# Performance work log

Hardware: AMD Instinct MI355X
Metric: run time of the kernel (lower is better)

Reference implementation:

```python
import jax, jax.numpy as jnp
import numpy as np

N = 50000        # nodes
E = 1250000      # edges
B = 512          # graphs
DIN, DH, DOUT = 64, 64, 16


def setup_inputs() -> dict:
    key = jax.random.key(0)
    ks = jax.random.split(key, 8)
    s = lambda d: np.float32(1.0 / np.sqrt(d))
    return {
        "x": jax.random.normal(ks[0], (N, DIN), jnp.float32),
        "edge_index": jax.random.randint(ks[1], (2, E), 0, N, dtype=jnp.int32),
        "batch": jnp.sort(jax.random.randint(ks[2], (N,), 0, B, dtype=jnp.int32)),
        "W1": jax.random.normal(ks[3], (DH, DIN), jnp.float32) * s(DIN),
        "b1": jnp.zeros((DH,), jnp.float32),
        "W2": jax.random.normal(ks[4], (DH, DH), jnp.float32) * s(DH),
        "b2": jnp.zeros((DH,), jnp.float32),
        "W3": jax.random.normal(ks[5], (DH, DH), jnp.float32) * s(DH),
        "b3": jnp.zeros((DH,), jnp.float32),
        "Wl": jax.random.normal(ks[6], (DOUT, DH), jnp.float32) * s(DH),
        "bl": jnp.zeros((DOUT,), jnp.float32),
    }


def _gcn_conv(x, src, dst, norm, W, b, n):
    # PyG GCNConv: h = x W^T; out[i] = sum_{(j->i)} norm_ji * h[j] + b
    h = x @ W.T                                   # [N, DH]
    msg = h[src] * norm[:, None]                  # [E+N, DH] gather
    return jax.ops.segment_sum(msg, dst, num_segments=n) + b


def reference(x, edge_index, batch, W1, b1, W2, b2, W3, b3, Wl, bl):
    n = x.shape[0]
    loop = jnp.arange(n, dtype=edge_index.dtype)
    # add self-loops (PyG GCNConv default add_self_loops=True)
    src = jnp.concatenate([edge_index[0], loop])
    dst = jnp.concatenate([edge_index[1], loop])
    # symmetric normalization: deg^{-1/2}[src] * deg^{-1/2}[dst]
    deg = jax.ops.segment_sum(jnp.ones_like(src, jnp.float32), dst, num_segments=n)
    dinv = jax.lax.rsqrt(deg)                     # deg >= 1 thanks to self-loops
    norm = dinv[src] * dinv[dst]

    h = x
    for W, b in ((W1, b1), (W2, b2), (W3, b3)):
        h = jax.nn.relu(_gcn_conv(h, src, dst, norm, W, b, n))

    # global mean pool over each graph
    sums = jax.ops.segment_sum(h, batch, num_segments=B)          # [B, DH]
    cnts = jax.ops.segment_sum(jnp.ones((n,), jnp.float32), batch, num_segments=B)
    pooled = sums / jnp.maximum(cnts, 1.0)[:, None]
    # dropout p=0.5 is identity in eval mode
    return pooled @ Wl.T + bl                                     # [B, DOUT]
```

## Files before the change

### kernel.cpp

```cpp
#include <hip/hip_runtime.h>
#include <hip/hip_fp16.h>


#define CAPB 3072
#define BINTILE 4096

__global__ __launch_bounds__(256) void init_kernel(int* __restrict__ fctr,
                                                   const int* __restrict__ batch,
                                                   const float* __restrict__ bl,
                                                   float* __restrict__ invc,
                                                   float* __restrict__ out,
                                                   int n, int nb) {
    int t = blockIdx.x * blockDim.x + threadIdx.x;
    if (t < 512) fctr[t] = 0;
    if (t < nb) {
        int l = 0, r = n;
        while (l < r) { int m = (l + r) >> 1; if (batch[m] < t) l = m + 1; else r = m; }
        int lo = l;
        r = n;
        while (l < r) { int m = (l + r) >> 1; if (batch[m] < t + 1) l = m + 1; else r = m; }
        invc[t] = 1.0f / fmaxf((float)(l - lo), 1.0f);
#pragma unroll
        for (int o = 0; o < 16; ++o) out[t * 16 + o] = bl[o];
    }
}

__global__ __launch_bounds__(256) void bin512_kernel(const int* __restrict__ src,
                                                     const int* __restrict__ dst,
                                                     int* __restrict__ fctr,
                                                     int2* __restrict__ recs2,
                                                     int e, int n) {
    __shared__ int lcnt[512], gbase[512];
    int tid = threadIdx.x;
    int s0  = blockIdx.x * BINTILE;
    lcnt[tid] = 0;
    lcnt[tid + 256] = 0;
    __syncthreads();
    int dv[16], bk[16];
#pragma unroll
    for (int k = 0; k < 16; ++k) {
        int i = s0 + tid + k * 256;
        if (i < e) {
            dv[k] = dst[i];
            bk[k] = (int)((512LL * dv[k]) / n);
            atomicAdd(&lcnt[bk[k]], 1);
        } else {
            bk[k] = -1;
        }
    }
    __syncthreads();
#pragma unroll
    for (int j = 0; j < 2; ++j) {
        int b = tid + j * 256;
        gbase[b] = b * CAPB + atomicAdd(&fctr[b], lcnt[b]);
        lcnt[b]  = 0;
    }
    __syncthreads();
#pragma unroll
    for (int k = 0; k < 16; ++k) {
        if (bk[k] >= 0) {
            int i = s0 + tid + k * 256;
            int p = gbase[bk[k]] + atomicAdd(&lcnt[bk[k]], 1);
            if (p < (bk[k] + 1) * CAPB) recs2[p] = make_int2(src[i], dv[k]);
        }
    }
}

__global__ __launch_bounds__(256) void sortfill_mm_kernel(
    const int2* __restrict__ recs2, const int* __restrict__ fctr,
    int* __restrict__ rp, float* __restrict__ dinv, int* __restrict__ csr,
    const float* __restrict__ x, const float* __restrict__ W1,
    __half* __restrict__ t1, int n) {
    __shared__ int hist[128];
    __shared__ int lofs[129];
    __shared__ int stage[CAPB];
    __shared__ int redbuf[256];
    __shared__ float xrow[98 * 64];
    int g   = blockIdx.x;
    int N0  = (int)(((long long)n * g + 511) / 512);
    int N1  = (int)(((long long)n * (g + 1) + 511) / 512);
    int nn  = N1 - N0;
    int tid = threadIdx.x;
    int lane = tid & 63;
    int wave = tid >> 6;

    int partial = 0;
    for (int j = tid; j < g; j += 256) partial += min(fctr[j], CAPB);
    redbuf[tid] = partial;
    if (tid < 128) hist[tid] = 0;
    __syncthreads();
    for (int s = 128; s > 0; s >>= 1) {
        if (tid < s) redbuf[tid] += redbuf[tid + s];
        __syncthreads();
    }
    int base = redbuf[0];
    const int2* my = recs2 + (size_t)g * CAPB;
    int total = min(fctr[g], CAPB);
    for (int i = tid; i < total; i += 256)
        atomicAdd(&hist[my[i].y - N0], 1);
    __syncthreads();
    if (tid == 0) {
        int acc = 0;
        for (int k = 0; k < nn; ++k) { lofs[k] = acc; acc += hist[k]; }
        lofs[nn] = acc;
    }
    __syncthreads();
    if (tid < 128) hist[tid] = 0;
    __syncthreads();
    for (int i = tid; i < total; i += 256) {
        int2 rec = my[i];
        int  li  = rec.y - N0;
        int  pos = lofs[li] + atomicAdd(&hist[li], 1);
        stage[pos] = rec.x;
    }
    __syncthreads();
    for (int j = tid; j < total; j += 256) csr[base + j] = stage[j];
    if (tid < nn) {
        rp[N0 + tid]   = base + lofs[tid];
        int deg        = lofs[tid + 1] - lofs[tid];
        dinv[N0 + tid] = rsqrtf((float)(deg + 1));
    }
    if (g == 511 && tid == 0) rp[n] = base + total;

    for (int idx = tid; idx < nn * 16; idx += 256)
        ((float4*)xrow)[idx] = ((const float4*)(x + (size_t)N0 * 64))[idx];
    float4 wreg[16];
    const float4* W4 = (const float4*)(W1 + lane * 64);
#pragma unroll
    for (int q = 0; q < 16; ++q) wreg[q] = W4[q];
    __syncthreads();
    for (int li = wave; li < nn; li += 4) {
        float dv = rsqrtf((float)(lofs[li + 1] - lofs[li] + 1));
        const float4* row = (const float4*)(xrow + li * 64);
        float acc = 0.0f;
#pragma unroll
        for (int q = 0; q < 16; ++q) {
            float4 hv = row[q];
            acc += hv.x * wreg[q].x + hv.y * wreg[q].y +
                   hv.z * wreg[q].z + hv.w * wreg[q].w;
        }
        t1[(size_t)(N0 + li) * 64 + lane] = __float2half(acc * dv);
    }
}

__global__ __launch_bounds__(256) void mm_kernel(const float* __restrict__ h,
                                                 const float* __restrict__ W,
                                                 const float* __restrict__ dinv,
                                                 __half* __restrict__ t, int n) {
    __shared__ float hs[64 * 64];
    int tid  = threadIdx.x;
    int lane = tid & 63;
    int wave = tid >> 6;
    int base = blockIdx.x * 64;

    float4 wreg[16];
    const float4* W4 = (const float4*)(W + lane * 64);
#pragma unroll
    for (int q = 0; q < 16; ++q) wreg[q] = W4[q];

    int nrows = min(64, n - base);
    const float4* h4  = (const float4*)(h + (size_t)base * 64);
    float4*       hs4 = (float4*)hs;
    for (int idx = tid; idx < nrows * 16; idx += 256) hs4[idx] = h4[idx];
    __syncthreads();

    for (int r = wave * 16; r < wave * 16 + 16; ++r) {
        int i = base + r;
        if (i >= n) break;
        const float4* row = (const float4*)(hs + r * 64);
        float acc = 0.0f;
#pragma unroll
        for (int q = 0; q < 16; ++q) {
            float4 hv = row[q];
            acc += hv.x * wreg[q].x + hv.y * wreg[q].y +
                   hv.z * wreg[q].z + hv.w * wreg[q].w;
        }
        t[(size_t)i * 64 + lane] = __float2half(acc * dinv[i]);
    }
}

__global__ __launch_bounds__(256, 6) void agg_kernel(const __half* __restrict__ t,
                                                     const int* __restrict__ rp,
                                                     const int* __restrict__ cs,
                                                     const float* __restrict__ dinv,
                                                     const float* __restrict__ bias,
                                                     float* __restrict__ hout, int n) {
    int gw   = (blockIdx.x * blockDim.x + threadIdx.x) >> 6;
    int lane = threadIdx.x & 63;
    if (gw >= n) return;
    int i   = gw;
    int grp = lane >> 4;
    int fo  = (lane & 15) << 2;
    int beg = rp[i];
    int end = rp[i + 1];
    uint2 su = *(const uint2*)(t + (size_t)i * 64 + fo);
    float dv = dinv[i];
    float4 bv = *(const float4*)(bias + fo);

    int deg = end - beg;
    int len = (deg + 3) >> 2;
    int gb  = beg + grp * len;
    int ge  = min(gb + len, end);

    float4 aa[4];
    aa[0] = make_float4(0.f, 0.f, 0.f, 0.f);
    aa[1] = aa[0]; aa[2] = aa[0]; aa[3] = aa[0];
    for (int eb = gb; eb < ge; eb += 8) {
#pragma unroll
        for (int j = 0; j < 8; ++j) {
            int   ej = eb + j;
            int   ec = min(ej, end - 1);
            int   sj = cs[ec];
            uint2 u  = *(const uint2*)(t + (size_t)sj * 64 + fo);
            float m  = (ej < ge) ? 1.0f : 0.0f;
            float2 f0 = __half22float2(*(const __half2*)&u.x);
            float2 f1 = __half22float2(*(const __half2*)&u.y);
            aa[j & 3].x = fmaf(m, f0.x, aa[j & 3].x);
            aa[j & 3].y = fmaf(m, f0.y, aa[j & 3].y);
            aa[j & 3].z = fmaf(m, f1.x, aa[j & 3].z);
            aa[j & 3].w = fmaf(m, f1.y, aa[j & 3].w);
        }
    }
    float4 acc;
    acc.x = (aa[0].x + aa[1].x) + (aa[2].x + aa[3].x);
    acc.y = (aa[0].y + aa[1].y) + (aa[2].y + aa[3].y);
    acc.z = (aa[0].z + aa[1].z) + (aa[2].z + aa[3].z);
    acc.w = (aa[0].w + aa[1].w) + (aa[2].w + aa[3].w);
    acc.x += __shfl_xor(acc.x, 16, 64);
    acc.y += __shfl_xor(acc.y, 16, 64);
    acc.z += __shfl_xor(acc.z, 16, 64);
    acc.w += __shfl_xor(acc.w, 16, 64);
    acc.x += __shfl_xor(acc.x, 32, 64);
    acc.y += __shfl_xor(acc.y, 32, 64);
    acc.z += __shfl_xor(acc.z, 32, 64);
    acc.w += __shfl_xor(acc.w, 32, 64);
    if (grp == 0) {
        float2 s01 = __half22float2(*(const __half2*)&su.x);
        float2 s23 = __half22float2(*(const __half2*)&su.y);
        float4 o;
        o.x = fmaxf(fmaf(dv, acc.x + s01.x, bv.x), 0.0f);
        o.y = fmaxf(fmaf(dv, acc.y + s01.y, bv.y), 0.0f);
        o.z = fmaxf(fmaf(dv, acc.z + s23.x, bv.z), 0.0f);
        o.w = fmaxf(fmaf(dv, acc.w + s23.y, bv.w), 0.0f);
        *(float4*)(hout + (size_t)i * 64 + fo) = o;
    }
}

__global__ __launch_bounds__(256, 6) void aggfinal_kernel(const __half* __restrict__ t,
                                                          const int* __restrict__ rp,
                                                          const int* __restrict__ cs,
                                                          const float* __restrict__ dinv,
                                                          const float* __restrict__ bias,
                                                          const float* __restrict__ Wl,
                                                          const int* __restrict__ batch,
                                                          const float* __restrict__ invc,
                                                          float* __restrict__ out, int n) {
    int gw   = (blockIdx.x * blockDim.x + threadIdx.x) >> 6;
    int lane = threadIdx.x & 63;
    if (gw >= n) return;
    int i   = gw;
    int grp = lane >> 4;
    int fo  = (lane & 15) << 2;
    int beg = rp[i];
    int end = rp[i + 1];
    uint2 su = *(const uint2*)(t + (size_t)i * 64 + fo);
    float dv = dinv[i];
    float4 bv = *(const float4*)(bias + fo);

    int deg = end - beg;
    int len = (deg + 3) >> 2;
    int gb  = beg + grp * len;
    int ge  = min(gb + len, end);

    float4 aa[4];
    aa[0] = make_float4(0.f, 0.f, 0.f, 0.f);
    aa[1] = aa[0]; aa[2] = aa[0]; aa[3] = aa[0];
    for (int eb = gb; eb < ge; eb += 8) {
#pragma unroll
        for (int j = 0; j < 8; ++j) {
            int   ej = eb + j;
            int   ec = min(ej, end - 1);
            int   sj = cs[ec];
            uint2 u  = *(const uint2*)(t + (size_t)sj * 64 + fo);
            float m  = (ej < ge) ? 1.0f : 0.0f;
            float2 f0 = __half22float2(*(const __half2*)&u.x);
            float2 f1 = __half22float2(*(const __half2*)&u.y);
            aa[j & 3].x = fmaf(m, f0.x, aa[j & 3].x);
            aa[j & 3].y = fmaf(m, f0.y, aa[j & 3].y);
            aa[j & 3].z = fmaf(m, f1.x, aa[j & 3].z);
            aa[j & 3].w = fmaf(m, f1.y, aa[j & 3].w);
        }
    }
    float4 acc;
    acc.x = (aa[0].x + aa[1].x) + (aa[2].x + aa[3].x);
    acc.y = (aa[0].y + aa[1].y) + (aa[2].y + aa[3].y);
    acc.z = (aa[0].z + aa[1].z) + (aa[2].z + aa[3].z);
    acc.w = (aa[0].w + aa[1].w) + (aa[2].w + aa[3].w);
    acc.x += __shfl_xor(acc.x, 16, 64);
    acc.y += __shfl_xor(acc.y, 16, 64);
    acc.z += __shfl_xor(acc.z, 16, 64);
    acc.w += __shfl_xor(acc.w, 16, 64);
    acc.x += __shfl_xor(acc.x, 32, 64);
    acc.y += __shfl_xor(acc.y, 32, 64);
    acc.z += __shfl_xor(acc.z, 32, 64);
    acc.w += __shfl_xor(acc.w, 32, 64);

    float2 s01 = __half22float2(*(const __half2*)&su.x);
    float2 s23 = __half22float2(*(const __half2*)&su.y);
    float4 h4;
    h4.x = fmaxf(fmaf(dv, acc.x + s01.x, bv.x), 0.0f);
    h4.y = fmaxf(fmaf(dv, acc.y + s01.y, bv.y), 0.0f);
    h4.z = fmaxf(fmaf(dv, acc.z + s23.x, bv.z), 0.0f);
    h4.w = fmaxf(fmaf(dv, acc.w + s23.y, bv.w), 0.0f);

    float4 wl0 = *(const float4*)(Wl + (0 * 4 + grp) * 64 + fo);
    float4 wl1 = *(const float4*)(Wl + (1 * 4 + grp) * 64 + fo);
    float4 wl2 = *(const float4*)(Wl + (2 * 4 + grp) * 64 + fo);
    float4 wl3 = *(const float4*)(Wl + (3 * 4 + grp) * 64 + fo);
    float z0 = h4.x * wl0.x + h4.y * wl0.y + h4.z * wl0.z + h4.w * wl0.w;
    float z1 = h4.x * wl1.x + h4.y * wl1.y + h4.z * wl1.z + h4.w * wl1.w;
    float z2 = h4.x * wl2.x + h4.y * wl2.y + h4.z * wl2.z + h4.w * wl2.w;
    float z3 = h4.x * wl3.x + h4.y * wl3.y + h4.z * wl3.z + h4.w * wl3.w;
#pragma unroll
    for (int s = 1; s <= 8; s <<= 1) {
        z0 += __shfl_xor(z0, s, 64);
        z1 += __shfl_xor(z1, s, 64);
        z2 += __shfl_xor(z2, s, 64);
        z3 += __shfl_xor(z3, s, 64);
    }
    int m = lane & 15;
    if (m < 4) {
        int   b  = batch[i];
        float ic = invc[b];
        float zv = (m == 0) ? z0 : (m == 1) ? z1 : (m == 2) ? z2 : z3;
        atomicAdd(out + b * 16 + (m * 4 + grp), zv * ic);
    }
}

extern "C" void kernel_launch(void* const* d_in, const int* in_sizes, int n_in,
                              void* d_out, int out_size, void* d_ws, size_t ws_size,
                              hipStream_t stream) {
    const float* x    = (const float*)d_in[0];
    const int*   ei   = (const int*)d_in[1];
    const int*   batch= (const int*)d_in[2];
    const float* W1   = (const float*)d_in[3];
    const float* b1   = (const float*)d_in[4];
    const float* W2   = (const float*)d_in[5];
    const float* b2   = (const float*)d_in[6];
    const float* W3   = (const float*)d_in[7];
    const float* b3   = (const float*)d_in[8];
    const float* Wl   = (const float*)d_in[9];
    const float* bl   = (const float*)d_in[10];
    float* out = (float*)d_out;

    int n  = in_sizes[0] / 64;
    int e  = in_sizes[1] / 2;
    int nb = out_size / 16;

    const int* esrc = ei;
    const int* edst = ei + e;

    char* p = (char*)d_ws;
    auto carve = [&](size_t bytes) {
        char* r = p;
        p += (bytes + 255) & ~(size_t)255;
        return r;
    };
    size_t featBytes = (size_t)n * 64 * 4;
    size_t recsBytes = (size_t)512 * CAPB * 8;
    size_t bufBBytes = recsBytes > featBytes ? recsBytes : featBytes;

    float*  dinv = (float*)carve((size_t)n * 4);
    int*    rp   = (int*)  carve((size_t)(n + 1) * 4);
    int*    csr  = (int*)  carve((size_t)e * 4);
    __half* bufT = (__half*)carve((size_t)n * 64 * 2);
    float*  bufB = (float*)carve(bufBBytes);
    int*    fctr = (int*)  carve(512 * 4);
    float*  invc = (float*)carve((size_t)nb * 4);
    int2*   recs2 = (int2*)bufB;

    dim3 blk(256);
    int gBIN = (e + BINTILE - 1) / BINTILE;
    int gMM  = (n + 63) / 64;
    int gAGG = (n + 3) / 4;

    init_kernel<<<2, blk, 0, stream>>>(fctr, batch, bl, invc, out, n, nb);
    bin512_kernel<<<gBIN, blk, 0, stream>>>(esrc, edst, fctr, recs2, e, n);
    sortfill_mm_kernel<<<512, blk, 0, stream>>>(recs2, fctr, rp, dinv, csr,
                                                x, W1, bufT, n);
    agg_kernel<<<gAGG, blk, 0, stream>>>(bufT, rp, csr, dinv, b1, bufB, n);
    mm_kernel<<<gMM, blk, 0, stream>>>(bufB, W2, dinv, bufT, n);
    agg_kernel<<<gAGG, blk, 0, stream>>>(bufT, rp, csr, dinv, b2, bufB, n);
    mm_kernel<<<gMM, blk, 0, stream>>>(bufB, W3, dinv, bufT, n);
    aggfinal_kernel<<<gAGG, blk, 0, stream>>>(bufT, rp, csr, dinv, b3, Wl,
                                              batch, invc, out, n);
}
```

Before: 288.2 us.

## Fuse GCN aggregation with next-layer matmul via shared-memory tile

Replaces the separate agg and mm kernels for layers 1-2 with a single kernel that aggregates 32 nodes per 512-thread block, writes the ReLU output to shared memory, and immediately multiplies by the next weight matrix to produce the fp16 transformed features. This removes the fp32 intermediate round-trip through global memory and two kernel launches per layer. Each node is now handled by a 16-lane group instead of a full wave split four ways, so per-node edge parallelism drops, which can hurt load balance on high-degree nodes. It also adds a ping-pong fp16 buffer and gives the edge records their own workspace region.

After: 287.2 us. No clear change (-0.4%).

```diff
diff --git a/kernel.cpp b/kernel.cpp
--- a/kernel.cpp
+++ b/kernel.cpp
@@ -143,106 +143,91 @@
     }
 }
 
-__global__ __launch_bounds__(256) void mm_kernel(const float* __restrict__ h,
-                                                 const float* __restrict__ W,
-                                                 const float* __restrict__ dinv,
-                                                 __half* __restrict__ t, int n) {
-    __shared__ float hs[64 * 64];
+__global__ __launch_bounds__(512, 4) void aggmm_kernel(const __half* __restrict__ t,
+                                                       const int* __restrict__ rp,
+                                                       const int* __restrict__ cs,
+                                                       const float* __restrict__ dinv,
+                                                       const float* __restrict__ bias,
+                                                       const float* __restrict__ W,
+                                                       __half* __restrict__ tout, int n) {
+    __shared__ float hs[32 * 64];
+    __shared__ float dvs[32];
     int tid  = threadIdx.x;
     int lane = tid & 63;
     int wave = tid >> 6;
-    int base = blockIdx.x * 64;
+    int g    = lane >> 4;
+    int fo   = (lane & 15) << 2;
+    int base = blockIdx.x * 32;
+    int nl   = wave * 4 + g;
+    int i    = base + nl;
+
+    float4 a0 = make_float4(0.f, 0.f, 0.f, 0.f);
+    float4 a1 = a0;
+    float2 s01 = make_float2(0.f, 0.f), s23 = s01;
+    float  dv = 1.0f;
+
+    if (i < n) {
+        int beg = rp[i];
+        int end = rp[i + 1];
+        uint2 su = *(const uint2*)(t + (size_t)i * 64 + fo);
+        dv = dinv[i];
+        for (int eb = beg; eb < end; eb += 8) {
+#pragma unroll
+            for (int j = 0; j < 8; ++j) {
+                int   ej = eb + j;
+                int   ec = min(ej, end - 1);
+                int   sj = cs[ec];
+                uint2 u  = *(const uint2*)(t + (size_t)sj * 64 + fo);
+                float m  = (ej < end) ? 1.0f : 0.0f;
+                float2 f0 = __half22float2(*(const __half2*)&u.x);
+                float2 f1 = __half22float2(*(const __half2*)&u.y);
+                if (j & 1) {
+                    a1.x = fmaf(m, f0.x, a1.x);
+                    a1.y = fmaf(m, f0.y, a1.y);
+                    a1.z = fmaf(m, f1.x, a1.z);
+                    a1.w = fmaf(m, f1.y, a1.w);
+                } else {
+                    a0.x = fmaf(m, f0.x, a0.x);
+                    a0.y = fmaf(m, f0.y, a0.y);
+                    a0.z = fmaf(m, f1.x, a0.z);
+                    a0.w = fmaf(m, f1.y, a0.w);
+                }
+            }
+        }
+        s01 = __half22float2(*(const __half2*)&su.x);
+        s23 = __half22float2(*(const __half2*)&su.y);
+    }
+    if (i < n) {
+        float4 bv = *(const float4*)(bias + fo);
+        float4 h4;
+        h4.x = fmaxf(fmaf(dv, (a0.x + a1.x) + s01.x, bv.x), 0.0f);
+        h4.y = fmaxf(fmaf(dv, (a0.y + a1.y) + s01.y, bv.y), 0.0f);
+        h4.z = fmaxf(fmaf(dv, (a0.z + a1.z) + s23.x, bv.z), 0.0f);
+        h4.w = fmaxf(fmaf(dv, (a0.w + a1.w) + s23.y, bv.w), 0.0f);
+        *(float4*)(hs + nl * 64 + fo) = h4;
+        if ((lane & 15) == 0) dvs[nl] = dv;
+    }
+    __syncthreads();
 
     float4 wreg[16];
     const float4* W4 = (const float4*)(W + lane * 64);
 #pragma unroll
     for (int q = 0; q < 16; ++q) wreg[q] = W4[q];
-
-    int nrows = min(64, n - base);
-    const float4* h4  = (const float4*)(h + (size_t)base * 64);
-    float4*       hs4 = (float4*)hs;
-    for (int idx = tid; idx < nrows * 16; idx += 256) hs4[idx] = h4[idx];
-    __syncthreads();
-
-    for (int r = wave * 16; r < wave * 16 + 16; ++r) {
-        int i = base + r;
-        if (i >= n) break;
-        const float4* row = (const float4*)(hs + r * 64);
-        float acc = 0.0f;
-#pragma unroll
-        for (int q = 0; q < 16; ++q) {
-            float4 hv = row[q];
-            acc += hv.x * wreg[q].x + hv.y * wreg[q].y +
-                   hv.z * wreg[q].z + hv.w * wreg[q].w;
-        }
-        t[(size_t)i * 64 + lane] = __float2half(acc * dinv[i]);
-    }
-}
-
-__global__ __launch_bounds__(256, 6) void agg_kernel(const __half* __restrict__ t,
-                                                     const int* __restrict__ rp,
-                                                     const int* __restrict__ cs,
-                                                     const float* __restrict__ dinv,
-                                                     const float* __restrict__ bias,
-                                                     float* __restrict__ hout, int n) {
-    int gw   = (blockIdx.x * blockDim.x + threadIdx.x) >> 6;
-    int lane = threadIdx.x & 63;
-    if (gw >= n) return;
-    int i   = gw;
-    int grp = lane >> 4;
-    int fo  = (lane & 15) << 2;
-    int beg = rp[i];
-    int end = rp[i + 1];
-    uint2 su = *(const uint2*)(t + (size_t)i * 64 + fo);
-    float dv = dinv[i];
-    float4 bv = *(const float4*)(bias + fo);
-
-    int deg = end - beg;
-    int len = (deg + 3) >> 2;
-    int gb  = beg + grp * len;
-    int ge  = min(gb + len, end);
-
-    float4 aa[4];
-    aa[0] = make_float4(0.f, 0.f, 0.f, 0.f);
-    aa[1] = aa[0]; aa[2] = aa[0]; aa[3] = aa[0];
-    for (int eb = gb; eb < ge; eb += 8) {
-#pragma unroll
-        for (int j = 0; j < 8; ++j) {
-            int   ej = eb + j;
-            int   ec = min(ej, end - 1);
-            int   sj = cs[ec];
-            uint2 u  = *(const uint2*)(t + (size_t)sj * 64 + fo);
-            float m  = (ej < ge) ? 1.0f : 0.0f;
-            float2 f0 = __half22float2(*(const __half2*)&u.x);
-            float2 f1 = __half22float2(*(const __half2*)&u.y);
-            aa[j & 3].x = fmaf(m, f0.x, aa[j & 3].x);
-            aa[j & 3].y = fmaf(m, f0.y, aa[j & 3].y);
-            aa[j & 3].z = fmaf(m, f1.x, aa[j & 3].z);
-            aa[j & 3].w = fmaf(m, f1.y, aa[j & 3].w);
-        }
-    }
-    float4 acc;
-    acc.x = (aa[0].x + aa[1].x) + (aa[2].x + aa[3].x);
-    acc.y = (aa[0].y + aa[1].y) + (aa[2].y + aa[3].y);
-    acc.z = (aa[0].z + aa[1].z) + (aa[2].z + aa[3].z);
-    acc.w = (aa[0].w + aa[1].w) + (aa[2].w + aa[3].w);
-    acc.x += __shfl_xor(acc.x, 16, 64);
-    acc.y += __shfl_xor(acc.y, 16, 64);
-    acc.z += __shfl_xor(acc.z, 16, 64);
-    acc.w += __shfl_xor(acc.w, 16, 64);
-    acc.x += __shfl_xor(acc.x, 32, 64);
-    acc.y += __shfl_xor(acc.y, 32, 64);
-    acc.z += __shfl_xor(acc.z, 32, 64);
-    acc.w += __shfl_xor(acc.w, 32, 64);
-    if (grp == 0) {
-        float2 s01 = __half22float2(*(const __half2*)&su.x);
-        float2 s23 = __half22float2(*(const __half2*)&su.y);
-        float4 o;
-        o.x = fmaxf(fmaf(dv, acc.x + s01.x, bv.x), 0.0f);
-        o.y = fmaxf(fmaf(dv, acc.y + s01.y, bv.y), 0.0f);
-        o.z = fmaxf(fmaf(dv, acc.z + s23.x, bv.z), 0.0f);
-        o.w = fmaxf(fmaf(dv, acc.w + s23.y, bv.w), 0.0f);
-        *(float4*)(hout + (size_t)i * 64 + fo) = o;
+#pragma unroll
+    for (int rr = 0; rr < 4; ++rr) {
+        int r  = wave * 4 + rr;
+        int io = base + r;
+        if (io < n) {
+            const float4* row = (const float4*)(hs + r * 64);
+            float acc = 0.0f;
+#pragma unroll
+            for (int q = 0; q < 16; ++q) {
+                float4 hv = row[q];
+                acc += hv.x * wreg[q].x + hv.y * wreg[q].y +
+                       hv.z * wreg[q].z + hv.w * wreg[q].w;
+            }
+            tout[(size_t)io * 64 + lane] = __float2half(acc * dvs[r]);
+        }
     }
 }
 
@@ -366,32 +351,26 @@
         p += (bytes + 255) & ~(size_t)255;
         return r;
     };
-    size_t featBytes = (size_t)n * 64 * 4;
-    size_t recsBytes = (size_t)512 * CAPB * 8;
-    size_t bufBBytes = recsBytes > featBytes ? recsBytes : featBytes;
-
-    float*  dinv = (float*)carve((size_t)n * 4);
-    int*    rp   = (int*)  carve((size_t)(n + 1) * 4);
-    int*    csr  = (int*)  carve((size_t)e * 4);
-    __half* bufT = (__half*)carve((size_t)n * 64 * 2);
-    float*  bufB = (float*)carve(bufBBytes);
-    int*    fctr = (int*)  carve(512 * 4);
-    float*  invc = (float*)carve((size_t)nb * 4);
-    int2*   recs2 = (int2*)bufB;
+    float*  dinv  = (float*)carve((size_t)n * 4);
+    int*    rp    = (int*)  carve((size_t)(n + 1) * 4);
+    int*    csr   = (int*)  carve((size_t)e * 4);
+    __half* tA    = (__half*)carve((size_t)n * 64 * 2);
+    __half* tB    = (__half*)carve((size_t)n * 64 * 2);
+    int2*   recs2 = (int2*) carve((size_t)512 * CAPB * 8);
+    int*    fctr  = (int*)  carve(512 * 4);
+    float*  invc  = (float*)carve((size_t)nb * 4);
 
     dim3 blk(256);
     int gBIN = (e + BINTILE - 1) / BINTILE;
-    int gMM  = (n + 63) / 64;
+    int gFUS = (n + 31) / 32;
     int gAGG = (n + 3) / 4;
 
     init_kernel<<<2, blk, 0, stream>>>(fctr, batch, bl, invc, out, n, nb);
     bin512_kernel<<<gBIN, blk, 0, stream>>>(esrc, edst, fctr, recs2, e, n);
     sortfill_mm_kernel<<<512, blk, 0, stream>>>(recs2, fctr, rp, dinv, csr,
-                                                x, W1, bufT, n);
-    agg_kernel<<<gAGG, blk, 0, stream>>>(bufT, rp, csr, dinv, b1, bufB, n);
-    mm_kernel<<<gMM, blk, 0, stream>>>(bufB, W2, dinv, bufT, n);
-    agg_kernel<<<gAGG, blk, 0, stream>>>(bufT, rp, csr, dinv, b2, bufB, n);
-    mm_kernel<<<gMM, blk, 0, stream>>>(bufB, W3, dinv, bufT, n);
-    aggfinal_kernel<<<gAGG, blk, 0, stream>>>(bufT, rp, csr, dinv, b3, Wl,
+                                                x, W1, tA, n);
+    aggmm_kernel<<<gFUS, dim3(512), 0, stream>>>(tA, rp, csr, dinv, b1, W2, tB, n);
+    aggmm_kernel<<<gFUS, dim3(512), 0, stream>>>(tB, rp, csr, dinv, b2, W3, tA, n);
+    aggfinal_kernel<<<gAGG, blk, 0, stream>>>(tA, rp, csr, dinv, b3, Wl,
                                               batch, invc, out, n);
 }
```

## Fuse aggregation with next-layer matmul and split gathers by source half

Applied to the files above, without the earlier changes.

Replaces the separate agg and mm kernels with one aggmm kernel. Each 512-thread block aggregates 8 nodes, stages the ReLU output in shared memory, and applies the next weight matrix right away. This removes the fp32 intermediate write and read and two launches, and ping-pongs between two half-precision buffers. The gather loop makes two passes, each restricted to one half of the source nodes for cache locality, at the cost of redundant index loads and masked gathers. The final aggregation kernel also batches its index and feature loads ahead of the accumulation behind a scheduling barrier to raise memory-level parallelism.

New measurement: 440.7 us. 52.9% more time.

```diff
diff --git a/kernel.cpp b/kernel.cpp
--- a/kernel.cpp
+++ b/kernel.cpp
@@ -143,61 +143,31 @@
     }
 }
 
-__global__ __launch_bounds__(256) void mm_kernel(const float* __restrict__ h,
-                                                 const float* __restrict__ W,
-                                                 const float* __restrict__ dinv,
-                                                 __half* __restrict__ t, int n) {
-    __shared__ float hs[64 * 64];
+__global__ __launch_bounds__(512, 4) void aggmm_kernel(const __half* __restrict__ t,
+                                                       const int* __restrict__ rp,
+                                                       const int* __restrict__ cs,
+                                                       const float* __restrict__ dinv,
+                                                       const float* __restrict__ bias,
+                                                       const float* __restrict__ W,
+                                                       __half* __restrict__ tout, int n) {
+    __shared__ float hs[8 * 64];
     int tid  = threadIdx.x;
     int lane = tid & 63;
     int wave = tid >> 6;
-    int base = blockIdx.x * 64;
-
-    float4 wreg[16];
-    const float4* W4 = (const float4*)(W + lane * 64);
-#pragma unroll
-    for (int q = 0; q < 16; ++q) wreg[q] = W4[q];
-
-    int nrows = min(64, n - base);
-    const float4* h4  = (const float4*)(h + (size_t)base * 64);
-    float4*       hs4 = (float4*)hs;
-    for (int idx = tid; idx < nrows * 16; idx += 256) hs4[idx] = h4[idx];
-    __syncthreads();
-
-    for (int r = wave * 16; r < wave * 16 + 16; ++r) {
-        int i = base + r;
-        if (i >= n) break;
-        const float4* row = (const float4*)(hs + r * 64);
-        float acc = 0.0f;
-#pragma unroll
-        for (int q = 0; q < 16; ++q) {
-            float4 hv = row[q];
-            acc += hv.x * wreg[q].x + hv.y * wreg[q].y +
-                   hv.z * wreg[q].z + hv.w * wreg[q].w;
-        }
-        t[(size_t)i * 64 + lane] = __float2half(acc * dinv[i]);
-    }
-}
-
-__global__ __launch_bounds__(256, 6) void agg_kernel(const __half* __restrict__ t,
-                                                     const int* __restrict__ rp,
-                                                     const int* __restrict__ cs,
-                                                     const float* __restrict__ dinv,
-                                                     const float* __restrict__ bias,
-                                                     float* __restrict__ hout, int n) {
-    int gw   = (blockIdx.x * blockDim.x + threadIdx.x) >> 6;
-    int lane = threadIdx.x & 63;
-    if (gw >= n) return;
-    int i   = gw;
-    int grp = lane >> 4;
-    int fo  = (lane & 15) << 2;
-    int beg = rp[i];
-    int end = rp[i + 1];
-    uint2 su = *(const uint2*)(t + (size_t)i * 64 + fo);
-    float dv = dinv[i];
+    int grp  = lane >> 4;
+    int fo   = (lane & 15) << 2;
+    int base = blockIdx.x * 8;
+    int i    = base + wave;
+    int ii   = min(i, n - 1);
+
+    int beg = rp[ii];
+    int end = rp[ii + 1];
+    int deg = end - beg;
+
+    uint2 su = *(const uint2*)(t + (size_t)ii * 64 + fo);
+    float dv = dinv[ii];
     float4 bv = *(const float4*)(bias + fo);
 
-    int deg = end - beg;
     int len = (deg + 3) >> 2;
     int gb  = beg + grp * len;
     int ge  = min(gb + len, end);
@@ -205,20 +175,29 @@
     float4 aa[4];
     aa[0] = make_float4(0.f, 0.f, 0.f, 0.f);
     aa[1] = aa[0]; aa[2] = aa[0]; aa[3] = aa[0];
-    for (int eb = gb; eb < ge; eb += 8) {
-#pragma unroll
-        for (int j = 0; j < 8; ++j) {
-            int   ej = eb + j;
-            int   ec = min(ej, end - 1);
-            int   sj = cs[ec];
-            uint2 u  = *(const uint2*)(t + (size_t)sj * 64 + fo);
-            float m  = (ej < ge) ? 1.0f : 0.0f;
-            float2 f0 = __half22float2(*(const __half2*)&u.x);
-            float2 f1 = __half22float2(*(const __half2*)&u.y);
-            aa[j & 3].x = fmaf(m, f0.x, aa[j & 3].x);
-            aa[j & 3].y = fmaf(m, f0.y, aa[j & 3].y);
-            aa[j & 3].z = fmaf(m, f1.x, aa[j & 3].z);
-            aa[j & 3].w = fmaf(m, f1.y, aa[j & 3].w);
+
+    int hn = (n + 1) >> 1;
+#pragma unroll
+    for (int hf = 0; hf < 2; ++hf) {
+        int lo = hf * hn;
+        int hi = min(lo + hn, n);
+        for (int eb = gb; eb < ge; eb += 8) {
+#pragma unroll
+            for (int j = 0; j < 8; ++j) {
+                int  ej = eb + j;
+                int  ec = min(ej, end - 1);
+                int  sj = cs[ec];
+                bool ok = (ej < ge) && (sj >= lo) && (sj < hi);
+                int  sc = ok ? sj : lo;
+                uint2 u  = *(const uint2*)(t + (size_t)sc * 64 + fo);
+                float m  = ok ? 1.0f : 0.0f;
+                float2 f0 = __half22float2(*(const __half2*)&u.x);
+                float2 f1 = __half22float2(*(const __half2*)&u.y);
+                aa[j & 3].x = fmaf(m, f0.x, aa[j & 3].x);
+                aa[j & 3].y = fmaf(m, f0.y, aa[j & 3].y);
+                aa[j & 3].z = fmaf(m, f1.x, aa[j & 3].z);
+                aa[j & 3].w = fmaf(m, f1.y, aa[j & 3].w);
+            }
         }
     }
     float4 acc;
@@ -234,15 +213,33 @@
     acc.y += __shfl_xor(acc.y, 32, 64);
     acc.z += __shfl_xor(acc.z, 32, 64);
     acc.w += __shfl_xor(acc.w, 32, 64);
-    if (grp == 0) {
+
+    if (grp == 0 && i < n) {
         float2 s01 = __half22float2(*(const __half2*)&su.x);
         float2 s23 = __half22float2(*(const __half2*)&su.y);
-        float4 o;
-        o.x = fmaxf(fmaf(dv, acc.x + s01.x, bv.x), 0.0f);
-        o.y = fmaxf(fmaf(dv, acc.y + s01.y, bv.y), 0.0f);
-        o.z = fmaxf(fmaf(dv, acc.z + s23.x, bv.z), 0.0f);
-        o.w = fmaxf(fmaf(dv, acc.w + s23.y, bv.w), 0.0f);
-        *(float4*)(hout + (size_t)i * 64 + fo) = o;
+        float4 h4;
+        h4.x = fmaxf(fmaf(dv, acc.x + s01.x, bv.x), 0.0f);
+        h4.y = fmaxf(fmaf(dv, acc.y + s01.y, bv.y), 0.0f);
+        h4.z = fmaxf(fmaf(dv, acc.z + s23.x, bv.z), 0.0f);
+        h4.w = fmaxf(fmaf(dv, acc.w + s23.y, bv.w), 0.0f);
+        *(float4*)(hs + wave * 64 + fo) = h4;
+    }
+    __syncthreads();
+
+    float4 wreg[16];
+    const float4* W4 = (const float4*)(W + lane * 64);
+#pragma unroll
+    for (int q = 0; q < 16; ++q) wreg[q] = W4[q];
+    if (i < n) {
+        const float4* row = (const float4*)(hs + wave * 64);
+        float acc2 = 0.0f;
+#pragma unroll
+        for (int q = 0; q < 16; ++q) {
+            float4 hv = row[q];
+            acc2 += hv.x * wreg[q].x + hv.y * wreg[q].y +
+                    hv.z * wreg[q].z + hv.w * wreg[q].w;
+        }
+        tout[(size_t)i * 64 + lane] = __float2half(acc2 * dv);
     }
 }
 
@@ -276,15 +273,19 @@
     aa[0] = make_float4(0.f, 0.f, 0.f, 0.f);
     aa[1] = aa[0]; aa[2] = aa[0]; aa[3] = aa[0];
     for (int eb = gb; eb < ge; eb += 8) {
+        int sjv[8];
+#pragma unroll
+        for (int j = 0; j < 8; ++j) sjv[j] = cs[min(eb + j, end - 1)];
+        uint2 ub[8];
+#pragma unroll
+        for (int j = 0; j < 8; ++j)
+            ub[j] = *(const uint2*)(t + (size_t)sjv[j] * 64 + fo);
+        __builtin_amdgcn_sched_barrier(0);
 #pragma unroll
         for (int j = 0; j < 8; ++j) {
-            int   ej = eb + j;
-            int   ec = min(ej, end - 1);
-            int   sj = cs[ec];
-            uint2 u  = *(const uint2*)(t + (size_t)sj * 64 + fo);
-            float m  = (ej < ge) ? 1.0f : 0.0f;
-            float2 f0 = __half22float2(*(const __half2*)&u.x);
-            float2 f1 = __half22float2(*(const __half2*)&u.y);
+            float m  = (eb + j < ge) ? 1.0f : 0.0f;
+            float2 f0 = __half22float2(*(const __half2*)&ub[j].x);
+            float2 f1 = __half22float2(*(const __half2*)&ub[j].y);
             aa[j & 3].x = fmaf(m, f0.x, aa[j & 3].x);
             aa[j & 3].y = fmaf(m, f0.y, aa[j & 3].y);
             aa[j & 3].z = fmaf(m, f1.x, aa[j & 3].z);
@@ -366,32 +367,26 @@
         p += (bytes + 255) & ~(size_t)255;
         return r;
     };
-    size_t featBytes = (size_t)n * 64 * 4;
-    size_t recsBytes = (size_t)512 * CAPB * 8;
-    size_t bufBBytes = recsBytes > featBytes ? recsBytes : featBytes;
-
-    float*  dinv = (float*)carve((size_t)n * 4);
-    int*    rp   = (int*)  carve((size_t)(n + 1) * 4);
-    int*    csr  = (int*)  carve((size_t)e * 4);
-    __half* bufT = (__half*)carve((size_t)n * 64 * 2);
-    float*  bufB = (float*)carve(bufBBytes);
-    int*    fctr = (int*)  carve(512 * 4);
-    float*  invc = (float*)carve((size_t)nb * 4);
-    int2*   recs2 = (int2*)bufB;
+    float*  dinv  = (float*)carve((size_t)n * 4);
+    int*    rp    = (int*)  carve((size_t)(n + 1) * 4);
+    int*    csr   = (int*)  carve((size_t)e * 4);
+    __half* tA    = (__half*)carve((size_t)n * 64 * 2);
+    __half* tB    = (__half*)carve((size_t)n * 64 * 2);
+    int2*   recs2 = (int2*) carve((size_t)512 * CAPB * 8);
+    int*    fctr  = (int*)  carve(512 * 4);
+    float*  invc  = (float*)carve((size_t)nb * 4);
 
     dim3 blk(256);
     int gBIN = (e + BINTILE - 1) / BINTILE;
-    int gMM  = (n + 63) / 64;
+    int gFUS = (n + 7) / 8;
     int gAGG = (n + 3) / 4;
 
     init_kernel<<<2, blk, 0, stream>>>(fctr, batch, bl, invc, out, n, nb);
     bin512_kernel<<<gBIN, blk, 0, stream>>>(esrc, edst, fctr, recs2, e, n);
     sortfill_mm_kernel<<<512, blk, 0, stream>>>(recs2, fctr, rp, dinv, csr,
-                                                x, W1, bufT, n);
-    agg_kernel<<<gAGG, blk, 0, stream>>>(bufT, rp, csr, dinv, b1, bufB, n);
-    mm_kernel<<<gMM, blk, 0, stream>>>(bufB, W2, dinv, bufT, n);
-    agg_kernel<<<gAGG, blk, 0, stream>>>(bufT, rp, csr, dinv, b2, bufB, n);
-    mm_kernel<<<gMM, blk, 0, stream>>>(bufB, W3, dinv, bufT, n);
-    aggfinal_kernel<<<gAGG, blk, 0, stream>>>(bufT, rp, csr, dinv, b3, Wl,
+                                                x, W1, tA, n);
+    aggmm_kernel<<<gFUS, dim3(512), 0, stream>>>(tA, rp, csr, dinv, b1, W2, tB, n);
+    aggmm_kernel<<<gFUS, dim3(512), 0, stream>>>(tB, rp, csr, dinv, b2, W3, tA, n);
+    aggfinal_kernel<<<gAGG, blk, 0, stream>>>(tA, rp, csr, dinv, b3, Wl,
                                               batch, invc, out, n);
 }
```
